# Performance work log

Measured on AMD Instinct MI355X. Metric: run time of the kernel, lower is better.

Reference implementation:

```python
import jax, jax.numpy as jnp
import numpy as np

B, S, D = 4, 1024, 768
H = 12
K = 64            # max relative distance
R = 2 * K + 1     # number of relative buckets
DH = D // H       # per-head dim (k_dim and v_dim both == d_model here)


def setup_inputs() -> dict:
    key = jax.random.key(0)
    ks = jax.random.split(key, 14)
    s = 0.02
    return {
        "query": jax.random.normal(ks[0], (B, S, D), jnp.float32),
        "key":   jax.random.normal(ks[1], (B, S, D), jnp.float32),
        "value": jax.random.normal(ks[2], (B, S, D), jnp.float32),
        "WQ_w": jax.random.normal(ks[3], (D, D), jnp.float32) * s,
        "WQ_b": jnp.zeros((D,), jnp.float32),
        "WK_w": jax.random.normal(ks[4], (D, D), jnp.float32) * s,
        "WK_b": jnp.zeros((D,), jnp.float32),
        "WV_w": jax.random.normal(ks[5], (D, D), jnp.float32) * s,
        "WV_b": jnp.zeros((D,), jnp.float32),
        "WO_w": jax.random.normal(ks[6], (D, D), jnp.float32) * s,
        "WO_b": jnp.zeros((D,), jnp.float32),
        "embK": jax.random.normal(ks[7], (R, D), jnp.float32) * s,
        "embV": jax.random.normal(ks[8], (R, D), jnp.float32) * s,
    }


def _split_heads(x):  # [B,S,D] -> [B,H,S,DH]
    b, s, _ = x.shape
    return x.reshape(b, s, H, DH).transpose(0, 2, 1, 3)


def reference(query, key, value, WQ_w, WQ_b, WK_w, WK_b, WV_w, WV_b, WO_w, WO_b, embK, embV):
    Q = _split_heads(query @ WQ_w.T + WQ_b)   # [B,H,Sq,DH]
    Kt = _split_heads(key @ WK_w.T + WK_b)    # [B,H,Sk,DH]
    V = _split_heads(value @ WV_w.T + WV_b)   # [B,H,Sk,DH]

    Sq, Sk = Q.shape[2], Kt.shape[2]
    # clipped relative position bucket index, matching get_relative_matrix
    idx = jnp.clip(jnp.arange(Sk)[None, :] - jnp.arange(Sq)[:, None], -K, K) + K  # [Sq,Sk]
    qrows = jnp.arange(Sq)[:, None]

    # content scores
    qk = jnp.einsum('bhqd,bhkd->bhqk', Q, Kt)
    # relative-K scores: project Q onto all R buckets, then gather per (q,k).
    # Mathematically identical to einsum('bhqd,hqkd->bhqk', Q, gather(embK)).
    embK_h = embK.reshape(R, H, DH)
    rel_all = jnp.einsum('bhqd,rhd->bhqr', Q, embK_h)        # [B,H,Sq,R]
    rel_scores = rel_all[:, :, qrows, idx]                   # [B,H,Sq,Sk]

    scores = (qk + rel_scores) / jnp.sqrt(jnp.asarray(DH, jnp.float32))
    attn = jax.nn.softmax(scores, axis=-1)                   # [B,H,Sq,Sk]

    out = jnp.einsum('bhqk,bhkv->bhqv', attn, V)             # [B,H,Sq,DH]
    # relative-V: scatter attention mass into R buckets per query, then one GEMM.
    w = jnp.zeros((B, H, Sq, R), attn.dtype).at[:, :, qrows, idx].add(attn)
    embV_h = embV.reshape(R, H, DH)
    out = out + jnp.einsum('bhqr,rhv->bhqv', w, embV_h)

    out = out.transpose(0, 2, 1, 3).reshape(B, Sq, D)        # merge heads
    out = out @ WO_w.T + WO_b                                 # (dropout p=0 is identity)
    return out, attn
```

## Files before the change

kernel.cpp:

```cpp
#include <hip/hip_runtime.h>

typedef _Float16 f16;
typedef _Float16 f16x4 __attribute__((ext_vector_type(4)));
typedef _Float16 f16x8 __attribute__((ext_vector_type(8)));
typedef float    f32x4 __attribute__((ext_vector_type(4)));

#define DEV static __device__ __forceinline__

DEV f32x4 mfma16(f16x8 a, f16x8 b, f32x4 c) {
    return __builtin_amdgcn_mfma_f32_16x16x32_f16(a, b, c, 0, 0, 0);
}

DEV void gload16(const f16* g, f16* l) {
    __builtin_amdgcn_global_load_lds(
        (const __attribute__((address_space(1))) unsigned int*)g,
        (__attribute__((address_space(3))) unsigned int*)l,
        16, 0, 0);
}


struct ConvArgs {
    const float* src[8];
    f16*         dst[8];
};

__global__ __launch_bounds__(256) void k_convert(ConvArgs a) {
    const int seg[9] = {0, 786432, 1572864, 2359296, 2506752, 2654208,
                        2801664, 2949120, 2973888};
    for (int i = blockIdx.x * 256 + threadIdx.x; i < 2973888; i += gridDim.x * 256) {
        int s = 0;
        while (i >= seg[s + 1]) s++;
        const int j = i - seg[s];
        const float4 v = ((const float4*)a.src[s])[j];
        f16x4 o;
        o[0] = (f16)v.x; o[1] = (f16)v.y; o[2] = (f16)v.z; o[3] = (f16)v.w;
        ((f16x4*)a.dst[s])[j] = o;
    }
}

__global__ __launch_bounds__(256) void k_embvt(const float* __restrict__ embV,
                                               f16* __restrict__ dst) {
    const int idx = blockIdx.x * 256 + threadIdx.x;
    if (idx >= 12 * 64 * 160) return;
    const int r  = idx % 160;
    const int dh = (idx / 160) % 64;
    const int h  = idx / (160 * 64);
    float v = 0.f;
    if (r < 129) v = embV[r * 768 + h * 64 + dh];
    dst[idx] = (f16)v;
}

#define GEMM_TILE_BODY(X, W)                                                   \
    const int tid = threadIdx.x;                                               \
    const int w = tid >> 6, l = tid & 63, quad = l >> 4, l16 = l & 15;         \
    const int wr = w >> 1, wc = w & 1;                                         \
    const int rl = l >> 2, cc = l & 3;                                         \
    const int csrc = (cc ^ ((rl ^ (rl >> 2)) & 3)) * 8;                        \
    const f16* gA = (X) + (size_t)(m0 + w * 32 + rl) * 768 + csrc;             \
    const f16* gB = (W) + (size_t)(n0 + w * 32 + rl) * 768 + csrc;             \
    f16* lA0 = As + (w * 32) * 32;                                             \
    f16* lA1 = As + (w * 32 + 16) * 32;                                        \
    f16* lB0 = Bs + (w * 32) * 32;                                             \
    f16* lB1 = Bs + (w * 32 + 16) * 32;                                        \
    const int xsw = (quad ^ ((l16 ^ (l16 >> 2)) & 3)) * 8;                     \
    f32x4 acc[4][4] = {};                                                      \
    for (int k0 = 0; k0 < 768; k0 += 32) {                                     \
        __syncthreads();                                                       \
        gload16(gA + k0, lA0);                                                 \
        gload16(gA + k0 + 16 * 768, lA1);                                      \
        gload16(gB + k0, lB0);                                                 \
        gload16(gB + k0 + 16 * 768, lB1);                                      \
        __syncthreads();                                                       \
        f16x8 af[4], bf[4];                                                    \
        _Pragma("unroll") for (int i = 0; i < 4; i++)                          \
            af[i] = *(const f16x8*)(As + (wr * 64 + i * 16 + l16) * 32 + xsw); \
        _Pragma("unroll") for (int i = 0; i < 4; i++)                          \
            bf[i] = *(const f16x8*)(Bs + (wc * 64 + i * 16 + l16) * 32 + xsw); \
        _Pragma("unroll") for (int i = 0; i < 4; i++)                          \
            _Pragma("unroll") for (int j = 0; j < 4; j++)                      \
                acc[i][j] = mfma16(af[i], bf[j], acc[i][j]);                   \
    }

__global__ __launch_bounds__(256) void k_gemm_qkv(
    const f16* __restrict__ xq, const f16* __restrict__ xk, const f16* __restrict__ xv,
    const f16* __restrict__ wq, const f16* __restrict__ wk, const f16* __restrict__ wv,
    const float* __restrict__ bq, const float* __restrict__ bk, const float* __restrict__ bv,
    f16* __restrict__ Qh, f16* __restrict__ Kh, f16* __restrict__ Vt) {
    __shared__ __align__(16) f16 As[128 * 32];
    __shared__ __align__(16) f16 Bs[128 * 32];

    const int t  = blockIdx.y / 6;
    const int n0 = (blockIdx.y % 6) * 128;
    const int m0 = blockIdx.x * 128;
    const f16*   X    = (t == 0) ? xq : (t == 1) ? xk : xv;
    const f16*   W    = (t == 0) ? wq : (t == 1) ? wk : wv;
    const float* bias = (t == 0) ? bq : (t == 1) ? bk : bv;

    GEMM_TILE_BODY(X, W)

#pragma unroll
    for (int j = 0; j < 4; j++) {
        const int   nj = n0 + wc * 64 + j * 16 + l16;
        const float bb = bias[nj];
        const int   h = nj >> 6, dh = nj & 63;
#pragma unroll
        for (int i = 0; i < 4; i++) {
            const int mb = m0 + wr * 64 + i * 16 + quad * 4;
            const int b = mb >> 10, s = mb & 1023;
            if (t < 2) {
                f16* dst = (t == 0) ? Qh : Kh;
                const int base = ((b * 12 + h) * 1024 + s) * 64 + dh;
#pragma unroll
                for (int r = 0; r < 4; r++)
                    dst[base + r * 64] = (f16)(acc[i][j][r] + bb);
            } else {
                f16x4 pk;
#pragma unroll
                for (int r = 0; r < 4; r++) pk[r] = (f16)(acc[i][j][r] + bb);
                *(f16x4*)(Vt + ((b * 12 + h) * 64 + dh) * 1024 + s) = pk;
            }
        }
    }
}

__global__ __launch_bounds__(256) void k_gemm_out(
    const f16* __restrict__ Xin, const f16* __restrict__ Win,
    const float* __restrict__ bias, float* __restrict__ out) {
    __shared__ __align__(16) f16 As[128 * 32];
    __shared__ __align__(16) f16 Bs[128 * 32];

    const int n0 = blockIdx.y * 128;
    const int m0 = blockIdx.x * 128;

    GEMM_TILE_BODY(Xin, Win)

#pragma unroll
    for (int j = 0; j < 4; j++) {
        const int   nj = n0 + wc * 64 + j * 16 + l16;
        const float bb = bias[nj];
#pragma unroll
        for (int i = 0; i < 4; i++) {
            const int mb = m0 + wr * 64 + i * 16 + quad * 4;
#pragma unroll
            for (int r = 0; r < 4; r++)
                out[(size_t)(mb + r) * 768 + nj] = acc[i][j][r] + bb;
        }
    }
}

constexpr int SCP = 1032;

__global__ __launch_bounds__(256) void k_attn(
    const f16* __restrict__ Qh, const f16* __restrict__ Kh, const f16* __restrict__ Vt,
    const f16* __restrict__ embK, const f16* __restrict__ embVt,
    float* __restrict__ attn, f16* __restrict__ ctx) {
    __shared__ __align__(16) f16 sc[16 * SCP];
    __shared__ __align__(16) f16 relw[16 * 160];
    __shared__ float red[3][4][16];
    __shared__ float invs[16], tl0[16], tl1[16];

    const int qt = blockIdx.x, bh = blockIdx.y;
    const int b = bh / 12, h = bh % 12;
    const int q0 = qt * 16;
    const int tid = threadIdx.x;
    const int w = tid >> 6, l = tid & 63, quad = l >> 4, l16 = l & 15;

    const f16* Qb = Qh + (bh * 1024 + q0) * 64;
    const f16* Kb = Kh + bh * 1024 * 64;
    const f16* Vb = Vt + bh * 64 * 1024;

    const f16x8 qa0 = *(const f16x8*)(Qb + l16 * 64 + quad * 8);
    const f16x8 qa1 = *(const f16x8*)(Qb + l16 * 64 + 32 + quad * 8);

    for (int nf = w; nf < 9; nf += 4) {
        const int r0 = nf * 16;
        int rr = r0 + l16; if (rr > 128) rr = 128;
        const f16x8 b0 = *(const f16x8*)(embK + rr * 768 + h * 64 + quad * 8);
        const f16x8 b1 = *(const f16x8*)(embK + rr * 768 + h * 64 + 32 + quad * 8);
        f32x4 a = {};
        a = mfma16(qa0, b0, a);
        a = mfma16(qa1, b1, a);
#pragma unroll
        for (int r = 0; r < 4; r++)
            relw[(quad * 4 + r) * 160 + r0 + l16] = (f16)a[r];
    }
    __syncthreads();

    float rs[4] = {0.f, 0.f, 0.f, 0.f};
    float rt0[4] = {0.f, 0.f, 0.f, 0.f};
    float rt1[4] = {0.f, 0.f, 0.f, 0.f};
    for (int nf = 0; nf < 16; nf++) {
        const int kc = w * 256 + nf * 16;
        const f16x8 b0 = *(const f16x8*)(Kb + (kc + l16) * 64 + quad * 8);
        const f16x8 b1 = *(const f16x8*)(Kb + (kc + l16) * 64 + 32 + quad * 8);
        f32x4 a = {};
        a = mfma16(qa0, b0, a);
        a = mfma16(qa1, b1, a);
        const int kg = kc + l16;
#pragma unroll
        for (int r = 0; r < 4; r++) {
            const int row = quad * 4 + r;
            const int qg = q0 + row;
            int d = kg - qg;
            d = (d < -64) ? -64 : (d > 64) ? 64 : d;
            const float s = (a[r] + (float)relw[row * 160 + d + 64]) * 0.125f;
            const float e = __expf(s);
            sc[row * SCP + kg] = (f16)e;
            rs[r] += e;
            rt0[r] += (kg <= qg - 64) ? e : 0.f;
            rt1[r] += (kg >= qg + 64) ? e : 0.f;
        }
    }
#pragma unroll
    for (int r = 0; r < 4; r++)
        for (int o = 1; o < 16; o <<= 1) {
            rs[r]  += __shfl_xor(rs[r], o);
            rt0[r] += __shfl_xor(rt0[r], o);
            rt1[r] += __shfl_xor(rt1[r], o);
        }
    if (l16 == 0) {
#pragma unroll
        for (int r = 0; r < 4; r++) {
            red[0][w][quad * 4 + r] = rs[r];
            red[1][w][quad * 4 + r] = rt0[r];
            red[2][w][quad * 4 + r] = rt1[r];
        }
    }
    __syncthreads();
    if (tid < 16) {
        const float s = red[0][0][tid] + red[0][1][tid] + red[0][2][tid] + red[0][3][tid];
        invs[tid] = 1.f / s;
        tl0[tid] = red[1][0][tid] + red[1][1][tid] + red[1][2][tid] + red[1][3][tid];
        tl1[tid] = red[2][0][tid] + red[2][1][tid] + red[2][2][tid] + red[2][3][tid];
    }
    __syncthreads();

    {
        float* ab = attn + ((long)bh * 1024 + q0) * 1024;
#pragma unroll
        for (int rr = 0; rr < 4; rr++) {
            const int row = w * 4 + rr;
            const float inv = invs[row];
            const f16* p = sc + row * SCP;
            float* o = ab + (long)row * 1024;
#pragma unroll
            for (int jj = 0; jj < 4; jj++) {
                const int c = jj * 256 + l * 4;
                const f16x4 v = *(const f16x4*)(p + c);
                *(float4*)(o + c) = make_float4((float)v[0] * inv, (float)v[1] * inv,
                                                (float)v[2] * inv, (float)v[3] * inv);
            }
        }
    }
    for (int idx = tid; idx < 16 * 160; idx += 256) {
        const int row = idx / 160, r = idx - row * 160;
        float v = 0.f;
        if (r == 0) v = tl0[row];
        else if (r == 128) v = tl1[row];
        else if (r < 128) {
            const int col = q0 + row + r - 64;
            if (col >= 0 && col < 1024) v = (float)sc[row * SCP + col];
        }
        relw[idx] = (f16)v;
    }
    __syncthreads();

    {
        f32x4 a = {};
        const f16* vrow = Vb + (w * 16 + l16) * 1024;
        for (int ks = 0; ks < 32; ks++) {
            const f16x8 af = *(const f16x8*)(sc + l16 * SCP + ks * 32 + quad * 8);
            const f16x8 bf = *(const f16x8*)(vrow + ks * 32 + quad * 8);
            a = mfma16(af, bf, a);
        }
        const f16* erow = embVt + (h * 64 + w * 16 + l16) * 160;
#pragma unroll
        for (int ks = 0; ks < 5; ks++) {
            const f16x8 af = *(const f16x8*)(relw + l16 * 160 + ks * 32 + quad * 8);
            const f16x8 bf = *(const f16x8*)(erow + ks * 32 + quad * 8);
            a = mfma16(af, bf, a);
        }
#pragma unroll
        for (int r = 0; r < 4; r++) {
            const int row = quad * 4 + r;
            const int qg = q0 + row;
            ctx[(b * 1024 + qg) * 768 + h * 64 + w * 16 + l16] = (f16)(a[r] * invs[row]);
        }
    }
}

extern "C" void kernel_launch(void* const* d_in, const int* in_sizes, int n_in,
                              void* d_out, int out_size, void* d_ws, size_t ws_size,
                              hipStream_t stream) {
    const float* q_in = (const float*)d_in[0];
    const float* k_in = (const float*)d_in[1];
    const float* v_in = (const float*)d_in[2];
    const float* WQw  = (const float*)d_in[3];
    const float* WQb  = (const float*)d_in[4];
    const float* WKw  = (const float*)d_in[5];
    const float* WKb  = (const float*)d_in[6];
    const float* WVw  = (const float*)d_in[7];
    const float* WVb  = (const float*)d_in[8];
    const float* WOw  = (const float*)d_in[9];
    const float* WOb  = (const float*)d_in[10];
    const float* embK = (const float*)d_in[11];
    const float* embV = (const float*)d_in[12];

    char*  ws  = (char*)d_ws;
    size_t off = 0;
    auto nxt = [&](size_t n) {
        char* p = ws + off;
        off += (n + 255) & ~(size_t)255;
        return p;
    };
    f16* qb    = (f16*)nxt(3145728 * 2);
    f16* kb    = (f16*)nxt(3145728 * 2);
    f16* vb    = (f16*)nxt(3145728 * 2);
    f16* Wqb   = (f16*)nxt(589824 * 2);
    f16* Wkb   = (f16*)nxt(589824 * 2);
    f16* Wvb   = (f16*)nxt(589824 * 2);
    f16* Wob   = (f16*)nxt(589824 * 2);
    f16* embKb = (f16*)nxt(99072 * 2);
    f16* embVt = (f16*)nxt(122880 * 2);
    f16* Qh    = (f16*)nxt(3145728 * 2);
    f16* Kh    = (f16*)nxt(3145728 * 2);
    f16* Vt    = (f16*)nxt(3145728 * 2);
    f16* ctx   = (f16*)nxt(3145728 * 2);
    (void)ws_size; (void)in_sizes; (void)n_in; (void)out_size;

    ConvArgs ca;
    ca.src[0] = q_in; ca.src[1] = k_in; ca.src[2] = v_in;
    ca.src[3] = WQw;  ca.src[4] = WKw;  ca.src[5] = WVw;
    ca.src[6] = WOw;  ca.src[7] = embK;
    ca.dst[0] = qb;   ca.dst[1] = kb;   ca.dst[2] = vb;
    ca.dst[3] = Wqb;  ca.dst[4] = Wkb;  ca.dst[5] = Wvb;
    ca.dst[6] = Wob;  ca.dst[7] = embKb;

    k_convert<<<dim3(2048), dim3(256), 0, stream>>>(ca);
    k_embvt<<<dim3(480), dim3(256), 0, stream>>>(embV, embVt);
    k_gemm_qkv<<<dim3(32, 18), dim3(256), 0, stream>>>(
        qb, kb, vb, Wqb, Wkb, Wvb, WQb, WKb, WVb, Qh, Kh, Vt);
    float* attn = (float*)d_out + 3145728;
    k_attn<<<dim3(64, 48), dim3(256), 0, stream>>>(Qh, Kh, Vt, embKb, embVt, attn, ctx);
    k_gemm_out<<<dim3(32, 6), dim3(256), 0, stream>>>(ctx, Wob, WOb, (float*)d_out);
}
```

Measured before the change: 398.8 us.

## Transpose MFMA operands so each lane owns a query row, fast-path clipped buckets

The QK^T and relative-K MFMAs swap their operands, so each lane holds one query row and four consecutive keys. This makes the score and relw stores packed f16x4 writes and reduces the row-sum shuffles to two steps. Tiles that sit entirely beyond the clip distance use a precomputed per-row relative bias instead of per-element relw lookups. The exponential becomes exp2 with the 1/sqrt(d) scale folded into a log2e constant. This adds branch divergence risk and some subtle indexing for the boundary tiles.

Measured after the change: 396.7 us. No clear change (-0.5%).

```diff
diff --git a/kernel.cpp b/kernel.cpp
--- a/kernel.cpp
+++ b/kernel.cpp
@@ -175,56 +175,70 @@
     for (int nf = w; nf < 9; nf += 4) {
         const int r0 = nf * 16;
         int rr = r0 + l16; if (rr > 128) rr = 128;
-        const f16x8 b0 = *(const f16x8*)(embK + rr * 768 + h * 64 + quad * 8);
-        const f16x8 b1 = *(const f16x8*)(embK + rr * 768 + h * 64 + 32 + quad * 8);
+        const f16x8 eb0 = *(const f16x8*)(embK + rr * 768 + h * 64 + quad * 8);
+        const f16x8 eb1 = *(const f16x8*)(embK + rr * 768 + h * 64 + 32 + quad * 8);
         f32x4 a = {};
-        a = mfma16(qa0, b0, a);
-        a = mfma16(qa1, b1, a);
-#pragma unroll
-        for (int r = 0; r < 4; r++)
-            relw[(quad * 4 + r) * 160 + r0 + l16] = (f16)a[r];
+        a = mfma16(eb0, qa0, a);
+        a = mfma16(eb1, qa1, a);
+        f16x4 pk;
+#pragma unroll
+        for (int r = 0; r < 4; r++) pk[r] = (f16)a[r];
+        *(f16x4*)(relw + l16 * 160 + r0 + quad * 4) = pk;
     }
     __syncthreads();
 
-    float rs[4] = {0.f, 0.f, 0.f, 0.f};
-    float rt0[4] = {0.f, 0.f, 0.f, 0.f};
-    float rt1[4] = {0.f, 0.f, 0.f, 0.f};
+    const int qg = q0 + l16;
+    const float cLog = 0.18033688f;
+    const float rLo = (float)relw[l16 * 160]       * cLog;
+    const float rHi = (float)relw[l16 * 160 + 128] * cLog;
+    float rs = 0.f, rt0 = 0.f, rt1 = 0.f;
+    const int dbase = w * 256 + quad * 4 - qg;
     for (int nf = 0; nf < 16; nf++) {
         const int kc = w * 256 + nf * 16;
-        const f16x8 b0 = *(const f16x8*)(Kb + (kc + l16) * 64 + quad * 8);
-        const f16x8 b1 = *(const f16x8*)(Kb + (kc + l16) * 64 + 32 + quad * 8);
+        const f16x8 kf0 = *(const f16x8*)(Kb + (kc + l16) * 64 + quad * 8);
+        const f16x8 kf1 = *(const f16x8*)(Kb + (kc + l16) * 64 + 32 + quad * 8);
         f32x4 a = {};
-        a = mfma16(qa0, b0, a);
-        a = mfma16(qa1, b1, a);
-        const int kg = kc + l16;
-#pragma unroll
-        for (int r = 0; r < 4; r++) {
-            const int row = quad * 4 + r;
-            const int qg = q0 + row;
-            int d = kg - qg;
-            d = (d < -64) ? -64 : (d > 64) ? 64 : d;
-            const float s = (a[r] + (float)relw[row * 160 + d + 64]) * 0.125f;
-            const float e = __expf(s);
-            sc[row * SCP + kg] = (f16)e;
-            rs[r] += e;
-            rt0[r] += (kg <= qg - 64) ? e : 0.f;
-            rt1[r] += (kg >= qg + 64) ? e : 0.f;
-        }
-    }
-#pragma unroll
-    for (int r = 0; r < 4; r++)
-        for (int o = 1; o < 16; o <<= 1) {
-            rs[r]  += __shfl_xor(rs[r], o);
-            rt0[r] += __shfl_xor(rt0[r], o);
-            rt1[r] += __shfl_xor(rt1[r], o);
-        }
-    if (l16 == 0) {
-#pragma unroll
-        for (int r = 0; r < 4; r++) {
-            red[0][w][quad * 4 + r] = rs[r];
-            red[1][w][quad * 4 + r] = rt0[r];
-            red[2][w][quad * 4 + r] = rt1[r];
-        }
+        a = mfma16(kf0, qa0, a);
+        a = mfma16(kf1, qa1, a);
+        const int d0 = dbase + nf * 16;
+        float es[4];
+        if (d0 >= 64) {
+#pragma unroll
+            for (int r = 0; r < 4; r++)
+                es[r] = __builtin_amdgcn_exp2f(fmaf(a[r], cLog, rHi));
+            const float s4 = (es[0] + es[1]) + (es[2] + es[3]);
+            rs += s4; rt1 += s4;
+        } else if (d0 <= -67) {
+#pragma unroll
+            for (int r = 0; r < 4; r++)
+                es[r] = __builtin_amdgcn_exp2f(fmaf(a[r], cLog, rLo));
+            const float s4 = (es[0] + es[1]) + (es[2] + es[3]);
+            rs += s4; rt0 += s4;
+        } else {
+#pragma unroll
+            for (int r = 0; r < 4; r++) {
+                const int dr = d0 + r;
+                const int drc = (dr < -64) ? -64 : (dr > 64) ? 64 : dr;
+                const float rv = (float)relw[l16 * 160 + drc + 64] * cLog;
+                const float e = __builtin_amdgcn_exp2f(fmaf(a[r], cLog, rv));
+                es[r] = e;
+                rs += e;
+                rt0 += (dr <= -64) ? e : 0.f;
+                rt1 += (dr >= 64) ? e : 0.f;
+            }
+        }
+        f16x4 pk;
+#pragma unroll
+        for (int r = 0; r < 4; r++) pk[r] = (f16)es[r];
+        *(f16x4*)(sc + l16 * SCP + kc + quad * 4) = pk;
+    }
+    rs  += __shfl_xor(rs, 16);  rs  += __shfl_xor(rs, 32);
+    rt0 += __shfl_xor(rt0, 16); rt0 += __shfl_xor(rt0, 32);
+    rt1 += __shfl_xor(rt1, 16); rt1 += __shfl_xor(rt1, 32);
+    if (l < 16) {
+        red[0][w][l16] = rs;
+        red[1][w][l16] = rt0;
+        red[2][w][l16] = rt1;
     }
     __syncthreads();
     if (tid < 16) {
@@ -283,8 +297,8 @@
 #pragma unroll
         for (int r = 0; r < 4; r++) {
             const int row = quad * 4 + r;
-            const int qg = q0 + row;
-            ctx[(b * 1024 + qg) * 768 + h * 64 + w * 16 + l16] = (f16)(a[r] * invs[row]);
+            const int qg2 = q0 + row;
+            ctx[(b * 1024 + qg2) * 768 + h * 64 + w * 16 + l16] = (f16)(a[r] * invs[row]);
         }
     }
 }
```
